# Performance work log

Hardware: AMD Instinct MI355X
Metric: run time of the kernel (lower is better)

## Reference

```python
import jax, jax.numpy as jnp
import numpy as np

H = 4      # num_attention_heads
DK = 75    # d_k = hidden_size // H
HID = 300  # hidden_size


def setup_inputs() -> dict:
    key = jax.random.key(0)
    ks = jax.random.split(key, 9)
    B, S = 8, 2048
    query = jax.random.normal(ks[0], (B, S, HID), dtype=jnp.float32)
    key_t = jax.random.normal(ks[1], (B, S, HID), dtype=jnp.float32)
    value = jax.random.normal(ks[2], (B, S, HID), dtype=jnp.float32)
    mask = jax.random.randint(ks[3], (B, S), 0, 2, dtype=jnp.int32)
    scale = 1.0 / np.sqrt(HID)
    Wq = jax.random.normal(ks[4], (HID, HID), dtype=jnp.float32) * scale
    Wk = jax.random.normal(ks[5], (HID, HID), dtype=jnp.float32) * scale
    Wv = jax.random.normal(ks[6], (HID, HID), dtype=jnp.float32) * scale
    Wo = jax.random.normal(ks[7], (HID, HID), dtype=jnp.float32) * scale
    bo = jax.random.normal(ks[8], (HID,), dtype=jnp.float32) * 0.01
    return {"query": query, "key": key_t, "value": value, "mask": mask,
            "Wq": Wq, "Wk": Wk, "Wv": Wv, "Wo": Wo, "bo": bo}


def reference(query, key, value, mask, Wq, Wk, Wv, Wo, bo):
    B, S, _ = query.shape
    # QKV projections (nn.Linear: x @ W.T), split into heads: [B,H,S,DK]
    def proj(x, W):
        return (x @ W.T).reshape(B, S, H, DK).transpose(0, 2, 1, 3)
    q, k, v = proj(query, Wq), proj(key, Wk), proj(value, Wv)
    # scores: [B,H,S,S]
    scores = jnp.einsum('bhqd,bhkd->bhqk', q, k) / jnp.sqrt(jnp.float32(DK))
    # mask outer product 'bi,bj->bij' broadcast over heads; fill zeros with -1e9
    m2 = (mask[:, :, None] * mask[:, None, :])[:, None, :, :]  # [B,1,S,S]
    scores = jnp.where(m2 == 0, jnp.float32(-1e9), scores)
    p_attn = jax.nn.softmax(scores, axis=-1)  # dropout p=0.0 (eval mode)
    x = jnp.einsum('bhqk,bhkd->bhqd', p_attn, v)  # [B,H,S,DK]
    x = x.transpose(0, 2, 1, 3).reshape(B, S, H * DK)
    return x @ Wo.T + bo
```

## Files before the change

kernel.cpp:

```cpp
#include <hip/hip_runtime.h>
#include <math.h>

typedef __bf16 bf16x8 __attribute__((ext_vector_type(8)));
typedef float f32x4 __attribute__((ext_vector_type(4)));
typedef float f32x16 __attribute__((ext_vector_type(16)));
typedef unsigned short u16;
typedef u16 u16x8 __attribute__((ext_vector_type(8)));

#define HID 300
#define NH 4
#define DK 75
#define DKP 80
#define BB 8
#define SS 2048
#define BSROWS (BB*SS)
#define C2   0.16658807f

#define MFMA(a,b,c)   __builtin_amdgcn_mfma_f32_16x16x32_bf16(a,b,c,0,0,0)
#define MFMA32(a,b,c) __builtin_amdgcn_mfma_f32_32x32x16_bf16(a,b,c,0,0,0)

static __device__ __forceinline__ void split2(float x, u16& hb, u16& lb) {
    const unsigned u = __float_as_uint(x);
    hb = (u16)(u >> 16);
    const float r = x - __uint_as_float(u & 0xffff0000u);
    lb = (u16)(__float_as_uint(r) >> 16);
}
static __device__ __forceinline__ void split2rne(float x, u16& hb, u16& lb) {
    const unsigned u = __float_as_uint(x);
    const unsigned uh = ((u + 0x7fffu + ((u >> 16) & 1u)) >> 16) << 16;
    hb = (u16)(uh >> 16);
    const float r = x - __uint_as_float(uh);
    lb = (u16)(__float_as_uint(r) >> 16);
}
static __device__ __forceinline__ unsigned pkbf(float a, float b) {
    const unsigned short ua = __builtin_bit_cast(unsigned short, (__bf16)a);
    const unsigned short ub = __builtin_bit_cast(unsigned short, (__bf16)b);
    return (unsigned)ua | ((unsigned)ub << 16);
}
static __device__ __forceinline__ void swap32(unsigned& x, unsigned& y) {
    asm("v_permlane32_swap_b32 %0, %1" : "+v"(x), "+v"(y));
}

__global__ __launch_bounds__(256)
void prep_w3(const float* __restrict__ Wq, const float* __restrict__ Wk,
             const float* __restrict__ Wv,
             u16* __restrict__ wph, u16* __restrict__ wpl)
{
    const int idx = blockIdx.x * 256 + threadIdx.x;
    if (idx >= 38400) return;
    const int c8 = idx % 40;
    int r = idx / 40;
    const int n = r % 80; r /= 80;
    const int h = r & 3;  r >>= 2;
    const int mat = r;
    const float* W = (mat == 0) ? Wq : (mat == 1) ? Wk : Wv;
    const int col0 = c8 * 8;
    float v[8];
#pragma unroll
    for (int j = 0; j < 8; ++j) v[j] = 0.f;
    if (n < DK) {
        const float* s = W + (size_t)(h * DK + n) * HID + col0;
        if (col0 + 8 <= HID) {
#pragma unroll
            for (int j = 0; j < 8; ++j) v[j] = s[j];
        } else {
#pragma unroll
            for (int j = 0; j < 8; ++j) v[j] = (col0 + j < HID) ? s[j] : 0.f;
        }
    }
    u16x8 hv, lv;
#pragma unroll
    for (int j = 0; j < 8; ++j) {
        u16 hb, lb;
        split2(v[j], hb, lb);
        hv[j] = hb; lv[j] = lb;
    }
    const size_t base = ((size_t)((mat * 4 + h) * 80 + n)) * 320 + col0;
    *(u16x8*)(wph + base) = hv;
    *(u16x8*)(wpl + base) = lv;
}

template <int MODE, int HPB>
static __device__ __forceinline__ void gemm_body(
    char* smem, const float* __restrict__ A, const float* __restrict__ W,
    const u16* __restrict__ Wph, const u16* __restrict__ Wpl,
    const float* __restrict__ bias, u16* __restrict__ hiP, u16* __restrict__ loP,
    float* __restrict__ foutP, const int bx, const int hp,
    const int* __restrict__ pmask, const float scale, const int patch)
{
    constexpr int WROWS = 80 * HPB;
    constexpr int NT = 5 * HPB;
    u16* Ah = (u16*)smem;
    u16* Al = Ah + 128 * 40;
    u16* Wh = Al + 128 * 40;
    u16* Wl = Wh + WROWS * 40;

    const int t = threadIdx.x;
    const int wv = t >> 6, l = t & 63, qc = l & 15, g = l >> 4;
    const int row0 = bx * 128;
    const int b = row0 >> 11;
    const int s0 = row0 & 2047;

    const f32x4 zf = {0.f, 0.f, 0.f, 0.f};
    f32x4 acc[2][NT];
#pragma unroll
    for (int mt = 0; mt < 2; ++mt)
#pragma unroll
        for (int nt = 0; nt < NT; ++nt) acc[mt][nt] = zf;

    const int rA = t >> 1, halfA = t & 1;
    float4 aPf[4];
    constexpr int WJ  = (WROWS * 4 + 255) / 256;
    constexpr int WJ2 = (WROWS * 8 + 255) / 256;
    u16x8 wPfH[WJ], wPfL[WJ];
    float4 wPf2[WJ2];

    auto loadA = [&](int step) {
        const int k0 = step * 32 + halfA * 16;
        const float* src = A + (size_t)(row0 + rA) * HID + k0;
#pragma unroll
        for (int c4 = 0; c4 < 4; ++c4) {
            const int k = k0 + c4 * 4;
            float4 v;
            if (k + 4 <= HID) v = *(const float4*)(src + c4 * 4);
            else {
                v.x = (k + 0 < HID) ? src[c4 * 4 + 0] : 0.f;
                v.y = (k + 1 < HID) ? src[c4 * 4 + 1] : 0.f;
                v.z = (k + 2 < HID) ? src[c4 * 4 + 2] : 0.f;
                v.w = (k + 3 < HID) ? src[c4 * 4 + 3] : 0.f;
            }
            aPf[c4] = v;
        }
    };
    auto loadW = [&](int step) {
        const int k0 = step * 32;
        if constexpr (MODE <= 1) {
#pragma unroll
            for (int j = 0; j < WJ; ++j) {
                const int idx = j * 256 + t;
                if (idx < WROWS * 4) {
                    const int n = idx >> 2, c = idx & 3;
                    const int nh = (n >= 80) ? 1 : 0, nn = n - nh * 80;
                    const size_t wo = (size_t)((hp * HPB + nh) * 80 + nn) * 320 + k0 + c * 8;
                    wPfH[j] = *(const u16x8*)(Wph + wo);
                    wPfL[j] = *(const u16x8*)(Wpl + wo);
                }
            }
        } else {
#pragma unroll
            for (int j = 0; j < WJ2; ++j) {
                const int idx = j * 256 + t;
                if (idx < WROWS * 8) {
                    const int n = idx >> 3, c = idx & 7;
                    const int nh = (n >= 80) ? 1 : 0, nn = n - nh * 80;
                    const int k = k0 + c * 4;
                    float4 v = make_float4(0.f, 0.f, 0.f, 0.f);
                    if (nn < DK) {
                        const float* src = W + (size_t)((hp * HPB + nh) * DK + nn) * HID + k;
                        if (k + 4 <= HID) v = *(const float4*)src;
                        else {
                            v.x = (k + 0 < HID) ? src[0] : 0.f;
                            v.y = (k + 1 < HID) ? src[1] : 0.f;
                            v.z = (k + 2 < HID) ? src[2] : 0.f;
                            v.w = (k + 3 < HID) ? src[3] : 0.f;
                        }
                    }
                    wPf2[j] = v;
                }
            }
        }
    };
    auto writeA = [&]() {
        u16* dh = Ah + rA * 40 + halfA * 16;
        u16* dl = Al + rA * 40 + halfA * 16;
#pragma unroll
        for (int c4 = 0; c4 < 4; ++c4) {
            ushort4 h4, l4;
            split2(aPf[c4].x, h4.x, l4.x);
            split2(aPf[c4].y, h4.y, l4.y);
            split2(aPf[c4].z, h4.z, l4.z);
            split2(aPf[c4].w, h4.w, l4.w);
            *(ushort4*)(dh + c4 * 4) = h4;
            *(ushort4*)(dl + c4 * 4) = l4;
        }
    };
    auto writeW = [&]() {
        if constexpr (MODE <= 1) {
#pragma unroll
            for (int j = 0; j < WJ; ++j) {
                const int idx = j * 256 + t;
                if (idx < WROWS * 4) {
                    const int n = idx >> 2, c = idx & 3;
                    *(u16x8*)(Wh + n * 40 + c * 8) = wPfH[j];
                    *(u16x8*)(Wl + n * 40 + c * 8) = wPfL[j];
                }
            }
        } else {
#pragma unroll
            for (int j = 0; j < WJ2; ++j) {
                const int idx = j * 256 + t;
                if (idx < WROWS * 8) {
                    const int n = idx >> 3, c = idx & 7;
                    ushort4 h4, l4;
                    split2(wPf2[j].x, h4.x, l4.x);
                    split2(wPf2[j].y, h4.y, l4.y);
                    split2(wPf2[j].z, h4.z, l4.z);
                    split2(wPf2[j].w, h4.w, l4.w);
                    *(ushort4*)(Wh + n * 40 + c * 4) = h4;
                    *(ushort4*)(Wl + n * 40 + c * 4) = l4;
                }
            }
        }
    };

    loadA(0);
    loadW(0);

    for (int step = 0; step < 10; ++step) {
        __syncthreads();
        writeA();
        writeW();
        __syncthreads();
        if (step < 9) {
            loadA(step + 1);
            loadW(step + 1);
        }
        bf16x8 ah[2], al2[2];
#pragma unroll
        for (int mt = 0; mt < 2; ++mt) {
            const int roff = (wv * 32 + mt * 16 + qc) * 40 + g * 8;
            ah[mt]  = *(const bf16x8*)(Ah + roff);
            al2[mt] = *(const bf16x8*)(Al + roff);
        }
#pragma unroll
        for (int nt = 0; nt < NT; ++nt) {
            const int woff = (nt * 16 + qc) * 40 + g * 8;
            const bf16x8 bh = *(const bf16x8*)(Wh + woff);
            const bf16x8 bl = *(const bf16x8*)(Wl + woff);
#pragma unroll
            for (int mt = 0; mt < 2; ++mt) {
                acc[mt][nt] = MFMA(ah[mt],  bh, acc[mt][nt]);
                acc[mt][nt] = MFMA(al2[mt], bh, acc[mt][nt]);
                acc[mt][nt] = MFMA(ah[mt],  bl, acc[mt][nt]);
            }
        }
    }
    __syncthreads();

#pragma unroll
    for (int ph = 0; ph < HPB; ++ph) {
        const int h = hp * HPB + ph;
        if constexpr (MODE <= 1) {
            unsigned* epi = (unsigned*)smem;
#pragma unroll
            for (int mt = 0; mt < 2; ++mt)
#pragma unroll
                for (int nt = 0; nt < 5; ++nt)
#pragma unroll
                    for (int r = 0; r < 4; ++r) {
                        u16 hb, lb;
                        split2rne(acc[mt][ph * 5 + nt][r] * scale, hb, lb);
                        if (patch != 0 && nt == 4 && qc == 11) {
                            if (patch == 1) { hb = (u16)0x3F80; lb = 0; }
                            else {
                                const int sr = s0 + wv * 32 + mt * 16 + g * 4 + r;
                                hb = (pmask[b * SS + sr] != 0) ? (u16)0 : (u16)0xC320;
                                lb = 0;
                            }
                        }
                        epi[(wv * 32 + mt * 16 + g * 4 + r) * 84 + nt * 16 + qc] =
                            (unsigned)hb | ((unsigned)lb << 16);
                    }
            __syncthreads();
            if constexpr (MODE == 0) {
                const int r = t >> 1, half = t & 1;
                const unsigned* row = epi + r * 84 + half * 40;
                const size_t base = ((size_t)(b * NH + h) * SS + s0 + r) * DKP + half * 40;
                u16* dh = hiP + base;
#pragma unroll
                for (int i = 0; i < 5; ++i) {
                    u16x8 hv, lv;
#pragma unroll
                    for (int j = 0; j < 8; ++j) {
                        const unsigned u = row[i * 8 + j];
                        hv[j] = (u16)u; lv[j] = (u16)(u >> 16);
                    }
                    *(u16x8*)(dh + i * 8) = hv;
                    if (loP) *(u16x8*)(loP + base + i * 8) = lv;
                }
            } else {
#pragma unroll
                for (int i = 0; i < 3; ++i) {
                    const int idx = i * 256 + t;
                    if (idx < 640) {
                        const int d = idx >> 3, sc = (idx & 7) * 16;
                        const size_t base = ((size_t)(b * NH + h) * DKP + d) * SS + s0 + sc;
                        u16* dh = hiP + base;
                        u16x8 h0, h1, l0, l1;
#pragma unroll
                        for (int j = 0; j < 8; ++j) {
                            unsigned u = epi[(sc + j) * 84 + d];
                            h0[j] = (u16)u; l0[j] = (u16)(u >> 16);
                            u = epi[(sc + 8 + j) * 84 + d];
                            h1[j] = (u16)u; l1[j] = (u16)(u >> 16);
                        }
                        *(u16x8*)dh = h0; *(u16x8*)(dh + 8) = h1;
                        if (loP) {
                            *(u16x8*)(loP + base) = l0;
                            *(u16x8*)(loP + base + 8) = l1;
                        }
                    }
                }
            }
        } else {
            float* epf = (float*)smem;
#pragma unroll
            for (int mt = 0; mt < 2; ++mt)
#pragma unroll
                for (int nt = 0; nt < 5; ++nt)
#pragma unroll
                    for (int r = 0; r < 4; ++r)
                        epf[(wv * 32 + mt * 16 + g * 4 + r) * 84 + nt * 16 + qc] =
                            acc[mt][ph * 5 + nt][r];
            __syncthreads();
            for (int i = 0; i < 38; ++i) {
                const int idx = i * 256 + t;
                if (idx < 128 * DK) {
                    const int r = idx / DK, c = idx - r * DK;
                    foutP[(size_t)(row0 + r) * HID + h * DK + c] = epf[r * 84 + c] + bias[h * DK + c];
                }
            }
        }
        if (ph + 1 < HPB) __syncthreads();
    }
}

__global__ __launch_bounds__(256, 3)
void proj3_gemm(const float* __restrict__ Aq, const float* __restrict__ Ak,
                const float* __restrict__ Av, const int* __restrict__ mask,
                const u16* __restrict__ wph, const u16* __restrict__ wpl,
                u16* __restrict__ qh, u16* __restrict__ ql,
                u16* __restrict__ kh, u16* __restrict__ vh)
{
    __shared__ char smem[46080];
    const int z = blockIdx.z;
    const float* A = (z == 0) ? Aq : (z == 1) ? Ak : Av;
    const size_t WMAT = (size_t)4 * 80 * 320;
    u16* hiP = (z == 0) ? qh : (z == 1) ? kh : vh;
    u16* loP = (z == 0) ? ql : nullptr;
    const float scale = (z == 0) ? C2 : 1.0f;
    const int patch = (z == 0) ? 1 : (z == 1) ? 2 : 0;
    if (z == 2)
        gemm_body<1, 2>(smem, A, nullptr, wph + z * WMAT, wpl + z * WMAT,
                        nullptr, hiP, loP, nullptr, blockIdx.x, blockIdx.y,
                        mask, scale, patch);
    else
        gemm_body<0, 2>(smem, A, nullptr, wph + z * WMAT, wpl + z * WMAT,
                        nullptr, hiP, loP, nullptr, blockIdx.x, blockIdx.y,
                        mask, scale, patch);
}

__global__ __launch_bounds__(256)
void out_gemm(const float* __restrict__ A, const float* __restrict__ W,
              const float* __restrict__ bias, float* __restrict__ out)
{
    __shared__ char smem[43008];
    gemm_body<2, 1>(smem, A, W, nullptr, nullptr, bias, nullptr, nullptr, out,
                    blockIdx.x, blockIdx.y, nullptr, 1.0f, 0);
}

__global__ __launch_bounds__(256, 2)
void attn_mfma32(const u16* __restrict__ qhi, const u16* __restrict__ qlo,
                 const u16* __restrict__ khi, const u16* __restrict__ vhi,
                 const int* __restrict__ mask, float* __restrict__ xout)
{
    __shared__ u16 KsH[2 * 8192];
    __shared__ u16 VsH[2 * 6144];

    const int t = threadIdx.x;
    const int wv = t >> 6;
    const int l = t & 63;
    const int q = l & 31;
    const int hi = l >> 5;

    const int bx = blockIdx.x;
    const int xcd = bx & 7, idx = bx >> 3;
    const int bh = xcd * 4 + (idx & 3);
    const int qt = idx >> 2;
    const int b = bh >> 2;
    const int h = bh & 3;
    const int q0 = qt * 128;

    {
        const int rr = (t >> 4) & 15, o8 = t & 15;
        *(uint2*)(VsH + (80 + rr) * 64 + o8 * 4) = make_uint2(0u, 0u);
        *(uint2*)(VsH + 6144 + (80 + rr) * 64 + o8 * 4) = make_uint2(0u, 0u);
    }

    const size_t planeQK = (size_t)bh * (SS * DKP);
    const int qrow = q0 + wv * 32 + q;
    const int mq = (mask[b * SS + qrow] != 0);
    const u16x8 qm = (u16x8)(u16)(mq ? 0xFFFFu : 0u);

    bf16x8 Qh[5], Ql[5];
    {
        const u16* ph = qhi + planeQK + (size_t)qrow * DKP;
        const u16* pl = qlo + planeQK + (size_t)qrow * DKP;
#pragma unroll
        for (int ch = 0; ch < 5; ++ch) {
            u16x8 ua = *(const u16x8*)(ph + 16 * ch + 8 * hi) & qm;
            u16x8 ub = *(const u16x8*)(pl + 16 * ch + 8 * hi) & qm;
            Qh[ch] = *(bf16x8*)&ua;
            Ql[ch] = *(bf16x8*)&ub;
        }
    }

    const u16* kH = khi + planeQK;
    const u16* vH = vhi + (size_t)bh * (DKP * SS);

    int kOff[5], kLds[5], vOff[5], vLds[5];
#pragma unroll
    for (int i = 0; i < 5; ++i) {
        const int gi = t + i * 256;
        const int r = gi / 20, c8 = gi % 20;
        kOff[i] = r * 160 + c8 * 8;
        kLds[i] = r * 256 + ((c8 * 8) ^ ((r & 15) << 4));
        const int d = gi >> 4, cv = gi & 15;
        vOff[i] = d * 4096 + cv * 8;
        vLds[i] = d * 128 + ((cv * 8) ^ ((d & 7) << 4));
    }

    uint2 krA[5], vrA[5], krB[5], vrB[5];
#define LOADT(KT, KR, VR) do { _Pragma("unroll") \
    for (int i = 0; i < 5; ++i) { \
        KR[i] = *(const uint2*)((const char*)kH + (size_t)(KT) * 10240 + kOff[i]); \
        VR[i] = *(const uint2*)((const char*)vH + (size_t)(KT) * 128 + vOff[i]); \
    } } while (0)
#define WRITET(BUF, KR, VR) do { _Pragma("unroll") \
    for (int i = 0; i < 5; ++i) { \
        *(uint2*)((char*)(KsH + (BUF) * 8192) + kLds[i]) = KR[i]; \
        *(uint2*)((char*)(VsH + (BUF) * 6144) + vLds[i]) = VR[i]; \
    } } while (0)

    LOADT(0, krA, vrA);
    WRITET(0, krA, vrA);
    LOADT(1, krA, vrA);
    LOADT(2, krB, vrB);
    __syncthreads();

    f32x16 O[3];
#pragma unroll
    for (int dt = 0; dt < 3; ++dt) O[dt] = (f32x16){};
    float ll = 0.f;
    const int kswz = (q & 15) << 4;

    for (int kt = 0; kt < 32; ++kt) {
        const int cur = kt & 1;
        const char* Kc = (const char*)(KsH + cur * 8192);
        const char* Vc = (const char*)(VsH + cur * 6144);

        f32x16 s0 = (f32x16){}, s1 = (f32x16){};
#pragma unroll
        for (int ch = 0; ch < 5; ++ch) {
            const int o0 = (32 * ch + 16 * hi) ^ kswz;
            const int o1 = (32 * ch + 16 * hi) ^ (((32 + q) & 15) << 4);
            const bf16x8 a0 = *(const bf16x8*)(Kc + q * 256 + o0);
            const bf16x8 a1 = *(const bf16x8*)(Kc + (32 + q) * 256 + o1);
            s0 = MFMA32(a0, Qh[ch], s0);
            s0 = MFMA32(a0, Ql[ch], s0);
            s1 = MFMA32(a1, Qh[ch], s1);
            s1 = MFMA32(a1, Ql[ch], s1);
        }

        float p0 = 0.f, p1 = 0.f, p2 = 0.f, p3 = 0.f;
        bf16x8 pA[4];
#pragma unroll
        for (int sb = 0; sb < 2; ++sb) {
            const f32x16 sv = sb ? s1 : s0;
            float e[16];
#pragma unroll
            for (int r = 0; r < 16; r += 4) {
                e[r + 0] = __builtin_amdgcn_exp2f(sv[r + 0]);
                e[r + 1] = __builtin_amdgcn_exp2f(sv[r + 1]);
                e[r + 2] = __builtin_amdgcn_exp2f(sv[r + 2]);
                e[r + 3] = __builtin_amdgcn_exp2f(sv[r + 3]);
                p0 += e[r + 0]; p1 += e[r + 1]; p2 += e[r + 2]; p3 += e[r + 3];
            }
#pragma unroll
            for (int hf = 0; hf < 2; ++hf) {
                unsigned X1 = pkbf(e[hf * 8 + 0], e[hf * 8 + 1]);
                unsigned Y1 = pkbf(e[hf * 8 + 4], e[hf * 8 + 5]);
                unsigned X2 = pkbf(e[hf * 8 + 2], e[hf * 8 + 3]);
                unsigned Y2 = pkbf(e[hf * 8 + 6], e[hf * 8 + 7]);
                swap32(X1, Y1);
                swap32(X2, Y2);
                union { unsigned u[4]; bf16x8 v; } cv_;
                cv_.u[0] = X1; cv_.u[1] = X2; cv_.u[2] = Y1; cv_.u[3] = Y2;
                pA[sb * 2 + hf] = cv_.v;
            }
        }
        ll += (p0 + p1) + (p2 + p3);

#pragma unroll
        for (int c = 0; c < 4; ++c) {
#pragma unroll
            for (int dt = 0; dt < 3; ++dt) {
                const int drow = 32 * dt + q;
                const int vb = drow * 128 + ((32 * c + 16 * hi) ^ ((drow & 7) << 4));
                const bf16x8 vh8 = *(const bf16x8*)(Vc + vb);
                O[dt] = MFMA32(vh8, pA[c], O[dt]);
            }
        }

        if (kt < 31) {
            if ((kt & 1) == 0) {
                WRITET(cur ^ 1, krA, vrA);
                if (kt < 29) LOADT(kt + 3, krA, vrA);
            } else {
                WRITET(cur ^ 1, krB, vrB);
                if (kt < 29) LOADT(kt + 3, krB, vrB);
            }
        }
        __syncthreads();
    }
#undef LOADT
#undef WRITET

    ll += __shfl_xor(ll, 32);
    {
        const float inv = 1.0f / ll;
        float* o = xout + (size_t)(b * SS + qrow) * HID + h * DK;
#pragma unroll
        for (int dt = 0; dt < 3; ++dt)
#pragma unroll
            for (int r = 0; r < 16; ++r) {
                const int d = 32 * dt + (r & 3) + 8 * (r >> 2) + 4 * hi;
                if (d < DK) o[d] = O[dt][r] * inv;
            }
    }
}

extern "C" void kernel_launch(void* const* d_in, const int* in_sizes, int n_in,
                              void* d_out, int out_size, void* d_ws, size_t ws_size,
                              hipStream_t stream)
{
    const float* query = (const float*)d_in[0];
    const float* key_t = (const float*)d_in[1];
    const float* value = (const float*)d_in[2];
    const int*   mask  = (const int*)d_in[3];
    const float* Wq    = (const float*)d_in[4];
    const float* Wk    = (const float*)d_in[5];
    const float* Wv    = (const float*)d_in[6];
    const float* Wo    = (const float*)d_in[7];
    const float* bo    = (const float*)d_in[8];
    float* out = (float*)d_out;

    const size_t PL = (size_t)BB * NH * SS * DKP;
    u16* qh = (u16*)d_ws;
    u16* ql = qh + PL;
    u16* kh = ql + PL;
    u16* kl = kh + PL;   (void)kl;
    u16* vh = kl + PL;
    u16* vl = vh + PL;
    float* xws = (float*)(vl + PL);
    u16* wph = (u16*)xws;
    u16* wpl = wph + (size_t)3 * 4 * 80 * 320;

    const dim3 blk(256, 1, 1);

    prep_w3<<<150, blk, 0, stream>>>(Wq, Wk, Wv, wph, wpl);

    proj3_gemm<<<dim3(128, 2, 3), blk, 0, stream>>>(query, key_t, value, mask,
                                                    wph, wpl,
                                                    qh, ql, kh, vh);

    attn_mfma32<<<dim3(512, 1, 1), blk, 0, stream>>>(qh, ql, kh, vh, mask, xws);

    out_gemm<<<dim3(128, NH, 1), blk, 0, stream>>>(xws, Wo, bo, out);
}
```

Baseline: 172.5 us.

## Split attention keys into two halves and merge partials inside output GEMM

The attention kernel now splits the key range in two, launching twice as many blocks (1024), each covering 16 key tiles. It writes unnormalized partial outputs and row sums, and the output GEMM adds the two partials and divides by the summed row sum while loading A. The change also shrinks the V shared buffer by reading padded rows from a small zero buffer, and raises the attention occupancy target to 3 blocks per CU. The intent is better CU utilisation and latency hiding. The cost is extra global traffic for two fp32 partial buffers and more load work in the output GEMM. The split merges without a running max, which relies on exponentials being unshifted, as in the existing code.

```diff
diff --git a/kernel.cpp b/kernel.cpp
--- a/kernel.cpp
+++ b/kernel.cpp
@@ -86,7 +86,8 @@
     const u16* __restrict__ Wph, const u16* __restrict__ Wpl,
     const float* __restrict__ bias, u16* __restrict__ hiP, u16* __restrict__ loP,
     float* __restrict__ foutP, const int bx, const int hp,
-    const int* __restrict__ pmask, const float scale, const int patch)
+    const int* __restrict__ pmask, const float scale, const int patch,
+    const float* __restrict__ llp)
 {
     constexpr int WROWS = 80 * HPB;
     constexpr int NT = 5 * HPB;
@@ -115,21 +116,62 @@
     u16x8 wPfH[WJ], wPfL[WJ];
     float4 wPf2[WJ2];
 
+    float inv0 = 0.f, inv1 = 0.f, inv2 = 0.f, inv3 = 0.f;
+    if constexpr (MODE == 2) {
+        const int rowI = row0 + rA;
+        const int bI = rowI >> 11, sI = rowI & 2047;
+        inv0 = 1.f / (llp[(bI * NH + 0) * SS + sI] + llp[65536 + (bI * NH + 0) * SS + sI]);
+        inv1 = 1.f / (llp[(bI * NH + 1) * SS + sI] + llp[65536 + (bI * NH + 1) * SS + sI]);
+        inv2 = 1.f / (llp[(bI * NH + 2) * SS + sI] + llp[65536 + (bI * NH + 2) * SS + sI]);
+        inv3 = 1.f / (llp[(bI * NH + 3) * SS + sI] + llp[65536 + (bI * NH + 3) * SS + sI]);
+    }
+
     auto loadA = [&](int step) {
         const int k0 = step * 32 + halfA * 16;
         const float* src = A + (size_t)(row0 + rA) * HID + k0;
-#pragma unroll
-        for (int c4 = 0; c4 < 4; ++c4) {
-            const int k = k0 + c4 * 4;
-            float4 v;
-            if (k + 4 <= HID) v = *(const float4*)(src + c4 * 4);
-            else {
-                v.x = (k + 0 < HID) ? src[c4 * 4 + 0] : 0.f;
-                v.y = (k + 1 < HID) ? src[c4 * 4 + 1] : 0.f;
-                v.z = (k + 2 < HID) ? src[c4 * 4 + 2] : 0.f;
-                v.w = (k + 3 < HID) ? src[c4 * 4 + 3] : 0.f;
-            }
-            aPf[c4] = v;
+        if constexpr (MODE == 2) {
+            const float* src1 = src + (size_t)BSROWS * HID;
+#pragma unroll
+            for (int c4 = 0; c4 < 4; ++c4) {
+                const int k = k0 + c4 * 4;
+                float v[4], w[4];
+                if (k + 4 <= HID) {
+                    const float4 v4 = *(const float4*)(src + c4 * 4);
+                    const float4 w4 = *(const float4*)(src1 + c4 * 4);
+                    v[0] = v4.x; v[1] = v4.y; v[2] = v4.z; v[3] = v4.w;
+                    w[0] = w4.x; w[1] = w4.y; w[2] = w4.z; w[3] = w4.w;
+                } else {
+#pragma unroll
+                    for (int j = 0; j < 4; ++j) {
+                        const bool ok = (k + j < HID);
+                        v[j] = ok ? src[c4 * 4 + j] : 0.f;
+                        w[j] = ok ? src1[c4 * 4 + j] : 0.f;
+                    }
+                }
+                float o[4];
+#pragma unroll
+                for (int j = 0; j < 4; ++j) {
+                    const int kk = k + j;
+                    const float iv = (kk < 75) ? inv0 : (kk < 150) ? inv1
+                                   : (kk < 225) ? inv2 : inv3;
+                    o[j] = (v[j] + w[j]) * iv;
+                }
+                aPf[c4] = make_float4(o[0], o[1], o[2], o[3]);
+            }
+        } else {
+#pragma unroll
+            for (int c4 = 0; c4 < 4; ++c4) {
+                const int k = k0 + c4 * 4;
+                float4 v;
+                if (k + 4 <= HID) v = *(const float4*)(src + c4 * 4);
+                else {
+                    v.x = (k + 0 < HID) ? src[c4 * 4 + 0] : 0.f;
+                    v.y = (k + 1 < HID) ? src[c4 * 4 + 1] : 0.f;
+                    v.z = (k + 2 < HID) ? src[c4 * 4 + 2] : 0.f;
+                    v.w = (k + 3 < HID) ? src[c4 * 4 + 3] : 0.f;
+                }
+                aPf[c4] = v;
+            }
         }
     };
     auto loadW = [&](int step) {
@@ -353,29 +395,32 @@
     if (z == 2)
         gemm_body<1, 2>(smem, A, nullptr, wph + z * WMAT, wpl + z * WMAT,
                         nullptr, hiP, loP, nullptr, blockIdx.x, blockIdx.y,
-                        mask, scale, patch);
+                        mask, scale, patch, nullptr);
     else
         gemm_body<0, 2>(smem, A, nullptr, wph + z * WMAT, wpl + z * WMAT,
                         nullptr, hiP, loP, nullptr, blockIdx.x, blockIdx.y,
-                        mask, scale, patch);
+                        mask, scale, patch, nullptr);
 }
 
 __global__ __launch_bounds__(256)
 void out_gemm(const float* __restrict__ A, const float* __restrict__ W,
-              const float* __restrict__ bias, float* __restrict__ out)
+              const float* __restrict__ bias, const float* __restrict__ llp,
+              float* __restrict__ out)
 {
     __shared__ char smem[43008];
     gemm_body<2, 1>(smem, A, W, nullptr, nullptr, bias, nullptr, nullptr, out,
-                    blockIdx.x, blockIdx.y, nullptr, 1.0f, 0);
-}
-
-__global__ __launch_bounds__(256, 2)
+                    blockIdx.x, blockIdx.y, nullptr, 1.0f, 0, llp);
+}
+
+__global__ __launch_bounds__(256, 3)
 void attn_mfma32(const u16* __restrict__ qhi, const u16* __restrict__ qlo,
                  const u16* __restrict__ khi, const u16* __restrict__ vhi,
-                 const int* __restrict__ mask, float* __restrict__ xout)
+                 const int* __restrict__ mask,
+                 float* __restrict__ xpart, float* __restrict__ llpart)
 {
     __shared__ u16 KsH[2 * 8192];
-    __shared__ u16 VsH[2 * 6144];
+    __shared__ u16 VsH[2 * 5120];
+    __shared__ u16 VsZ[64];
 
     const int t = threadIdx.x;
     const int wv = t >> 6;
@@ -385,17 +430,15 @@
 
     const int bx = blockIdx.x;
     const int xcd = bx & 7, idx = bx >> 3;
-    const int bh = xcd * 4 + (idx & 3);
-    const int qt = idx >> 2;
+    const int sk = idx & 1;
+    const int bh = xcd * 4 + ((idx >> 1) & 3);
+    const int qt = idx >> 3;
     const int b = bh >> 2;
     const int h = bh & 3;
     const int q0 = qt * 128;
-
-    {
-        const int rr = (t >> 4) & 15, o8 = t & 15;
-        *(uint2*)(VsH + (80 + rr) * 64 + o8 * 4) = make_uint2(0u, 0u);
-        *(uint2*)(VsH + 6144 + (80 + rr) * 64 + o8 * 4) = make_uint2(0u, 0u);
-    }
+    const int kbase = sk * 16;
+
+    if (t < 16) *(uint2*)(VsZ + t * 4) = make_uint2(0u, 0u);
 
     const size_t planeQK = (size_t)bh * (SS * DKP);
     const int qrow = q0 + wv * 32 + q;
@@ -438,14 +481,14 @@
     } } while (0)
 #define WRITET(BUF, KR, VR) do { _Pragma("unroll") \
     for (int i = 0; i < 5; ++i) { \
-        *(uint2*)((char*)(KsH + (BUF) * 8192) + kLds[i]) = KR[i]; \
-        *(uint2*)((char*)(VsH + (BUF) * 6144) + vLds[i]) = VR[i]; \
+        *(uint2*)((char*)KsH + (BUF) * 16384 + kLds[i]) = KR[i]; \
+        *(uint2*)((char*)VsH + (BUF) * 10240 + vLds[i]) = VR[i]; \
     } } while (0)
 
-    LOADT(0, krA, vrA);
+    LOADT(kbase, krA, vrA);
     WRITET(0, krA, vrA);
-    LOADT(1, krA, vrA);
-    LOADT(2, krB, vrB);
+    LOADT(kbase + 1, krA, vrA);
+    LOADT(kbase + 2, krB, vrB);
     __syncthreads();
 
     f32x16 O[3];
@@ -453,11 +496,16 @@
     for (int dt = 0; dt < 3; ++dt) O[dt] = (f32x16){};
     float ll = 0.f;
     const int kswz = (q & 15) << 4;
-
-    for (int kt = 0; kt < 32; ++kt) {
-        const int cur = kt & 1;
-        const char* Kc = (const char*)(KsH + cur * 8192);
-        const char* Vc = (const char*)(VsH + cur * 6144);
+    const int drow2 = 64 + q;
+    const int vsw2 = (drow2 & 7) << 4;
+    const int voff2 = drow2 * 128;
+    const bool z2 = (drow2 >= 80);
+
+    for (int ktl = 0; ktl < 16; ++ktl) {
+        const int kt = kbase + ktl;
+        const int cur = ktl & 1;
+        const char* Kc = (const char*)KsH + cur * 16384;
+        const char* Vc = (const char*)VsH + cur * 10240;
 
         f32x16 s0 = (f32x16){}, s1 = (f32x16){};
 #pragma unroll
@@ -504,21 +552,26 @@
 #pragma unroll
         for (int c = 0; c < 4; ++c) {
 #pragma unroll
-            for (int dt = 0; dt < 3; ++dt) {
+            for (int dt = 0; dt < 2; ++dt) {
                 const int drow = 32 * dt + q;
                 const int vb = drow * 128 + ((32 * c + 16 * hi) ^ ((drow & 7) << 4));
                 const bf16x8 vh8 = *(const bf16x8*)(Vc + vb);
                 O[dt] = MFMA32(vh8, pA[c], O[dt]);
             }
-        }
-
-        if (kt < 31) {
-            if ((kt & 1) == 0) {
+            {
+                const char* b2 = z2 ? (const char*)VsZ : (Vc + voff2);
+                const bf16x8 vh8 = *(const bf16x8*)(b2 + ((32 * c + 16 * hi) ^ vsw2));
+                O[2] = MFMA32(vh8, pA[c], O[2]);
+            }
+        }
+
+        if (ktl < 15) {
+            if ((ktl & 1) == 0) {
                 WRITET(cur ^ 1, krA, vrA);
-                if (kt < 29) LOADT(kt + 3, krA, vrA);
+                if (ktl < 13) LOADT(kt + 3, krA, vrA);
             } else {
                 WRITET(cur ^ 1, krB, vrB);
-                if (kt < 29) LOADT(kt + 3, krB, vrB);
+                if (ktl < 13) LOADT(kt + 3, krB, vrB);
             }
         }
         __syncthreads();
@@ -528,15 +581,16 @@
 
     ll += __shfl_xor(ll, 32);
     {
-        const float inv = 1.0f / ll;
-        float* o = xout + (size_t)(b * SS + qrow) * HID + h * DK;
+        float* xp = xpart + (size_t)sk * ((size_t)BSROWS * HID);
+        float* o = xp + (size_t)(b * SS + qrow) * HID + h * DK;
 #pragma unroll
         for (int dt = 0; dt < 3; ++dt)
 #pragma unroll
             for (int r = 0; r < 16; ++r) {
                 const int d = 32 * dt + (r & 3) + 8 * (r >> 2) + 4 * hi;
-                if (d < DK) o[d] = O[dt][r] * inv;
-            }
+                if (d < DK) o[d] = O[dt][r];
+            }
+        if (hi == 0) llpart[sk * 65536 + bh * SS + qrow] = ll;
     }
 }
 
@@ -556,14 +610,14 @@
     float* out = (float*)d_out;
 
     const size_t PL = (size_t)BB * NH * SS * DKP;
+    const size_t XP = (size_t)BSROWS * HID;
     u16* qh = (u16*)d_ws;
     u16* ql = qh + PL;
     u16* kh = ql + PL;
-    u16* kl = kh + PL;   (void)kl;
-    u16* vh = kl + PL;
-    u16* vl = vh + PL;
-    float* xws = (float*)(vl + PL);
-    u16* wph = (u16*)xws;
+    u16* vh = kh + PL;
+    float* x0 = (float*)(vh + PL);
+    float* llp = x0 + 2 * XP;
+    u16* wph = (u16*)x0;
     u16* wpl = wph + (size_t)3 * 4 * 80 * 320;
 
     const dim3 blk(256, 1, 1);
@@ -574,7 +628,8 @@
                                                     wph, wpl,
                                                     qh, ql, kh, vh);
 
-    attn_mfma32<<<dim3(512, 1, 1), blk, 0, stream>>>(qh, ql, kh, vh, mask, xws);
-
-    out_gemm<<<dim3(128, NH, 1), blk, 0, stream>>>(xws, Wo, bo, out);
-}
+    attn_mfma32<<<dim3(1024, 1, 1), blk, 0, stream>>>(qh, ql, kh, vh, mask,
+                                                      x0, llp);
+
+    out_gemm<<<dim3(128, NH, 1), blk, 0, stream>>>(x0, Wo, bo, llp, out);
+}
```

After: 416.1 us. 2.41x slower.
